# Optimization experiments

Hardware: AMD Instinct MI355X
Metric: run time of the kernel (lower is better)

The kernel has to match this reference:

```python
import jax, jax.numpy as jnp
import numpy as np
from jax import lax

B, CIN, CH, HW, K = 256, 256, 256, 16, 3


def setup_inputs() -> dict:
    key = jax.random.key(0)
    ks = jax.random.split(key, 9)
    s = 0.05
    return {
        "x": jax.random.normal(ks[0], (B, CIN, HW, HW), dtype=jnp.float32),
        "h": jax.random.normal(ks[1], (B, CH, HW, HW), dtype=jnp.float32),
        "c": jax.random.normal(ks[2], (B, CH, HW, HW), dtype=jnp.float32),
        # stacked x-branch conv weights for gates [i, f, c, o]; no bias (matches torch code)
        "Wx": jax.random.normal(ks[3], (4 * CH, CIN, K, K), dtype=jnp.float32) * s,
        # stacked h-branch conv weights for gates [i, f, c, o]; with bias
        "Wh": jax.random.normal(ks[4], (4 * CH, CH, K, K), dtype=jnp.float32) * s,
        "bh": jax.random.normal(ks[5], (4 * CH,), dtype=jnp.float32) * s,
        # peephole params (torch inits them to zeros; use small randn to exercise the math)
        "Wci": jax.random.normal(ks[6], (1, CH, HW, HW), dtype=jnp.float32) * s,
        "Wcf": jax.random.normal(ks[7], (1, CH, HW, HW), dtype=jnp.float32) * s,
        "Wco": jax.random.normal(ks[8], (1, CH, HW, HW), dtype=jnp.float32) * s,
    }


def _conv(x, w):
    # same-padding 2D conv, NCHW/OIHW
    return lax.conv_general_dilated(
        x, w, window_strides=(1, 1), padding="SAME",
        dimension_numbers=("NCHW", "OIHW", "NCHW"))


def reference(x, h, c, Wx, Wh, bh, Wci, Wcf, Wco):
    gx = _conv(x, Wx)                                   # [B, 4*CH, H, W]
    gh = _conv(h, Wh) + bh[None, :, None, None]         # [B, 4*CH, H, W]
    xi, xf, xc, xo = jnp.split(gx, 4, axis=1)
    hi, hf, hc, ho = jnp.split(gh, 4, axis=1)
    i_t = jax.nn.sigmoid(xi + hi + Wci * c)
    f_t = jax.nn.sigmoid(xf + hf + Wcf * c)
    c_t = f_t * c + i_t * jnp.tanh(xc + hc)
    o_t = jax.nn.sigmoid(xo + ho + Wco * c_t)
    h_t = o_t * jnp.tanh(c_t)
    return (h_t, c_t)
```

## Files before the change

kernel.cpp:

```cpp
#include <hip/hip_runtime.h>


typedef __bf16 bf16x8 __attribute__((ext_vector_type(8)));
typedef float f32x16 __attribute__((ext_vector_type(16)));

#define PLANE_B  20736u
#define XH_BYTES (4096u * PLANE_B)
#define OUT_HALF 16777216u

__device__ inline void gload_lds16(const void* g, void* l) {
    __builtin_amdgcn_global_load_lds(
        (const __attribute__((address_space(1))) void*)g,
        (__attribute__((address_space(3))) void*)l, 16, 0, 0);
}

__global__ __launch_bounds__(256) void xh_transform(
    const float* __restrict__ x, const float* __restrict__ hh,
    unsigned char* __restrict__ xh)
{
    int blk = blockIdx.x;
    int b = blk >> 4, ibk = blk & 15;
    const float* src = (ibk < 8) ? (x  + ((size_t)(b*256 + ibk*32)) * 256)
                                 : (hh + ((size_t)(b*256 + (ibk-8)*32)) * 256);
    int t = threadIdx.x;
    uint32_t w[16];
#pragma unroll
    for (int i = 0; i < 16; ++i) {
        __bf16 lo = (__bf16)src[(size_t)(2*i  )*256 + t];
        __bf16 hi = (__bf16)src[(size_t)(2*i+1)*256 + t];
        w[i] = (uint32_t)__builtin_bit_cast(unsigned short, lo)
             | ((uint32_t)__builtin_bit_cast(unsigned short, hi) << 16);
    }
    unsigned char* plane = xh + (size_t)blk * PLANE_B;
    int p = ((t >> 4) + 1)*18 + (t & 15) + 1;
    uint32_t key  = (uint32_t)(p & 7) << 4;
    uint32_t base = (uint32_t)p * 64u;
#pragma unroll
    for (int k = 0; k < 4; ++k)
        *(uint4*)(plane + ((base + 16u*k) ^ key)) =
            uint4{w[4*k], w[4*k+1], w[4*k+2], w[4*k+3]};
    if (t < 68) {
        int pb;
        if      (t < 18) pb = t;
        else if (t < 36) pb = 17*18 + (t - 18);
        else if (t < 52) pb = (t - 35)*18;
        else             pb = (t - 51)*18 + 17;
        uint32_t kb = (uint32_t)(pb & 7) << 4;
        uint32_t bb = (uint32_t)pb * 64u;
        uint4 z{0u,0u,0u,0u};
#pragma unroll
        for (int k = 0; k < 4; ++k)
            *(uint4*)(plane + ((bb + 16u*k) ^ kb)) = z;
    }
}

__global__ __launch_bounds__(256) void w_transform(
    const float* __restrict__ Wx, const float* __restrict__ Wh,
    __bf16* __restrict__ Wt)
{
    int idx  = blockIdx.x * 256 + threadIdx.x;
    int lane = idx & 63;
    int chunk = idx >> 6;
    int f    = chunk & 3;
    int half = (chunk >> 2) & 1;
    int pos  = (chunk >> 3) % 9;
    int rest = (chunk >> 3) / 9;
    int ibk  = rest & 15;
    int cb   = rest >> 4;
    int row = lane & 31, hl = lane >> 5;
    int gate = row & 3, ch8 = row >> 2;
    int oc  = gate*256 + cb*32 + f*8 + ch8;
    int ic0 = ibk*32 + half*16 + hl*8;
    bf16x8 v;
#pragma unroll
    for (int j = 0; j < 8; ++j) {
        int ic = ic0 + j;
        float w = (ic < 256) ? Wx[((size_t)oc*256 + ic      )*9 + pos]
                             : Wh[((size_t)oc*256 + (ic-256))*9 + pos];
        v[j] = (__bf16)w;
    }
    *(bf16x8*)(Wt + (size_t)chunk*512 + (size_t)lane*8) = v;
}

__global__ __launch_bounds__(256, 2) void convlstm_main(
    const unsigned char* __restrict__ xh, const unsigned char* __restrict__ Wtb,
    const float* __restrict__ bh,  const float* __restrict__ cin,
    const float* __restrict__ Wci, const float* __restrict__ Wcf,
    const float* __restrict__ Wco, float* __restrict__ out)
{
    int bid = blockIdx.x;
    int cb  = bid & 7;
    int b   = bid >> 3;
    int tid = threadIdx.x;
    int lane = tid & 63, wv = tid >> 6;
    int wm = wv & 1, wf = wv >> 1;
    int l31 = lane & 31, hl = lane >> 5;

    __shared__ __align__(16) unsigned char lds[2][24576];

    f32x16 acc[4][2];
#pragma unroll
    for (int j = 0; j < 2; ++j) {
        int fg = wf*2 + j;
        f32x16 v;
#pragma unroll
        for (int r = 0; r < 16; ++r) {
            int gate = r & 3, q = r >> 2;
            v[r] = bh[gate*256 + cb*32 + fg*8 + 2*q + hl];
        }
        acc[0][j] = v; acc[1][j] = v; acc[2][j] = v; acc[3][j] = v;
    }

    const unsigned char* planes = xh + (size_t)b * (16u * PLANE_B);

#pragma unroll
    for (int k = 0; k < 6; ++k)
        gload_lds16(planes + (size_t)(wv*6 + k)*1024u + (size_t)lane*16u,
                    &lds[0][(wv*6 + k)*1024 + lane*16]);

    int m0 = wm*128 + l31;
    int pb0 = (m0 >> 4)*18 + (m0 & 15);
    const uint32_t kbase = (uint32_t)(hl*16);
    uint32_t baddr[9][2];
#pragma unroll
    for (int pos = 0; pos < 9; ++pos) {
        int d = (pos/3)*18 + (pos%3);
        int pp = pb0 + d;
        uint32_t a = ((uint32_t)pp*64u + kbase) ^ (((uint32_t)(pp & 7)) << 4);
        baddr[pos][0] = a;
        baddr[pos][1] = (a + 2304u) ^ 64u;
    }
    const char* lds0 = (const char*)&lds[0][0];

    const unsigned char* aptr = Wtb + (size_t)cb*1179648u
                                    + (size_t)(wf*2048) + (size_t)(lane*16);

    bf16x8 A[3][2], Bb[2][4];
    A[0][0] = *(const bf16x8*)(aptr + 0);
    A[0][1] = *(const bf16x8*)(aptr + 1024);
    A[1][0] = *(const bf16x8*)(aptr + 4096);
    A[1][1] = *(const bf16x8*)(aptr + 5120);

    __syncthreads();

#define IBK_PHASES(LAST)                                                     \
    {                                                                        \
           \
        Bb[0][0] = *(const bf16x8*)(lds0 + baddr[0][0]);                     \
        Bb[0][1] = *(const bf16x8*)(lds0 + baddr[0][1]);                     \
        Bb[0][2] = *(const bf16x8*)(lds0 + baddr[0][0] + 4608);              \
        Bb[0][3] = *(const bf16x8*)(lds0 + baddr[0][1] + 4608);              \
        _Pragma("unroll")                                                    \
        for (int p = 0; p < 18; ++p) {                                       \
                                    \
            {                                                                \
                const int tp = p + 2;                                        \
                const int off = (tp < 18)                                    \
                    ? (tp*4096)                                              \
                    : ((LAST) ? (17*4096)                         \
                              : (73728 + (tp-18)*4096));                     \
                A[(p+2)%3][0] = *(const bf16x8*)(aptr + off);                \
                A[(p+2)%3][1] = *(const bf16x8*)(aptr + off + 1024);         \
            }                                                                \
            if (p == 1 && !(LAST)) {                                         \
                const unsigned char* np_ = planes + (size_t)(ibk+1)*PLANE_B; \
                _Pragma("unroll")                                            \
                for (int k = 0; k < 6; ++k)                                  \
                    gload_lds16(np_ + (size_t)(wv*6 + k)*1024u               \
                                    + (size_t)lane*16u,                      \
                                &lds[(ibk & 1) ^ 1][(wv*6 + k)*1024          \
                                                    + lane*16]);             \
            }                                                                \
                                \
            if (p < 17) {                                                    \
                const int np = p + 1;                                        \
                const uint32_t hx = (uint32_t)((np & 1)*32);                 \
                uint32_t a0 = baddr[np>>1][0] ^ hx;                          \
                uint32_t a1 = baddr[np>>1][1] ^ hx;                          \
                Bb[np&1][0] = *(const bf16x8*)(lds0 + a0);                   \
                Bb[np&1][1] = *(const bf16x8*)(lds0 + a1);                   \
                Bb[np&1][2] = *(const bf16x8*)(lds0 + a0 + 4608);            \
                Bb[np&1][3] = *(const bf16x8*)(lds0 + a1 + 4608);            \
            }                                                                \
            __builtin_amdgcn_s_setprio(1);                                   \
            acc[0][0] = __builtin_amdgcn_mfma_f32_32x32x16_bf16(A[p%3][0], Bb[p&1][0], acc[0][0], 0, 0, 0); \
            acc[0][1] = __builtin_amdgcn_mfma_f32_32x32x16_bf16(A[p%3][1], Bb[p&1][0], acc[0][1], 0, 0, 0); \
            acc[1][0] = __builtin_amdgcn_mfma_f32_32x32x16_bf16(A[p%3][0], Bb[p&1][1], acc[1][0], 0, 0, 0); \
            acc[1][1] = __builtin_amdgcn_mfma_f32_32x32x16_bf16(A[p%3][1], Bb[p&1][1], acc[1][1], 0, 0, 0); \
            acc[2][0] = __builtin_amdgcn_mfma_f32_32x32x16_bf16(A[p%3][0], Bb[p&1][2], acc[2][0], 0, 0, 0); \
            acc[2][1] = __builtin_amdgcn_mfma_f32_32x32x16_bf16(A[p%3][1], Bb[p&1][2], acc[2][1], 0, 0, 0); \
            acc[3][0] = __builtin_amdgcn_mfma_f32_32x32x16_bf16(A[p%3][0], Bb[p&1][3], acc[3][0], 0, 0, 0); \
            acc[3][1] = __builtin_amdgcn_mfma_f32_32x32x16_bf16(A[p%3][1], Bb[p&1][3], acc[3][1], 0, 0, 0); \
            __builtin_amdgcn_s_setprio(0);                                   \
        }                                                                    \
    }

    int flipd = 24576;
    for (int ibk = 0; ibk < 15; ++ibk) {
        IBK_PHASES(0)
#pragma unroll
        for (int pos = 0; pos < 9; ++pos) {
            baddr[pos][0] += (uint32_t)flipd;
            baddr[pos][1] += (uint32_t)flipd;
        }
        flipd = -flipd;
        aptr += 73728;
        asm volatile("s_waitcnt vmcnt(4) lgkmcnt(0)" ::: "memory");
        __builtin_amdgcn_s_barrier();
        __builtin_amdgcn_sched_barrier(0);
    }
    {
        const int ibk = 15;
        (void)ibk;
        IBK_PHASES(1)
    }
#undef IBK_PHASES

    float* outh = out;
    float* outc = out + (size_t)OUT_HALF;
    const size_t bOff = (size_t)b * (256*256);
#pragma unroll
    for (int mf = 0; mf < 4; ++mf) {
        int m = wm*128 + mf*32 + l31;
#pragma unroll
        for (int j = 0; j < 2; ++j) {
            int fg = wf*2 + j;
#pragma unroll
            for (int q = 0; q < 4; ++q) {
                int ch = cb*32 + fg*8 + 2*q + hl;
                size_t pidx = (size_t)ch*256 + (size_t)m;
                size_t idx  = bOff + pidx;
                float cv = cin[idx];
                float pi = acc[mf][j][4*q+0];
                float pf = acc[mf][j][4*q+1];
                float pc = acc[mf][j][4*q+2];
                float po = acc[mf][j][4*q+3];
                float it = 1.f/(1.f + __expf(-(pi + Wci[pidx]*cv)));
                float ft = 1.f/(1.f + __expf(-(pf + Wcf[pidx]*cv)));
                float tc = 1.f - 2.f/(1.f + __expf(2.f*pc));
                float ct = ft*cv + it*tc;
                float ot = 1.f/(1.f + __expf(-(po + Wco[pidx]*ct)));
                float th = 1.f - 2.f/(1.f + __expf(2.f*ct));
                outh[idx] = ot*th;
                outc[idx] = ct;
            }
        }
    }
}

extern "C" void kernel_launch(void* const* d_in, const int* in_sizes, int n_in,
                              void* d_out, int out_size, void* d_ws, size_t ws_size,
                              hipStream_t stream)
{
    const float* x   = (const float*)d_in[0];
    const float* h   = (const float*)d_in[1];
    const float* c   = (const float*)d_in[2];
    const float* Wx  = (const float*)d_in[3];
    const float* Wh  = (const float*)d_in[4];
    const float* bh  = (const float*)d_in[5];
    const float* Wci = (const float*)d_in[6];
    const float* Wcf = (const float*)d_in[7];
    const float* Wco = (const float*)d_in[8];
    float* out = (float*)d_out;

    unsigned char* xh = (unsigned char*)d_ws;
    unsigned char* wtb = xh + (size_t)XH_BYTES + 4096;

    hipLaunchKernelGGL(xh_transform, dim3(4096), dim3(256), 0, stream, x, h, xh);
    hipLaunchKernelGGL(w_transform,  dim3(2304), dim3(256), 0, stream,
                       Wx, Wh, (__bf16*)wtb);
    hipLaunchKernelGGL(convlstm_main, dim3(2048), dim3(256), 0, stream,
                       xh, wtb, bh, c, Wci, Wcf, Wco, out);
}
```

Measured before the change: 580.9 us.

## Triple-buffer LDS input planes and prefetch two iterations ahead

Grows the LDS staging from two plane buffers to three. Each input-channel block is now fetched two iterations ahead, and the first B fragments of the next block are read from LDS before the barrier. The end-of-iteration wait is relaxed to vmcnt(32) with no lgkmcnt drain, so the global-to-LDS copy latency has more time to hide behind MFMA work. The cost is 72KB of LDS per block, which leaves little headroom for two blocks per CU, plus more complex rotating buffer-offset bookkeeping.

```diff
diff --git a/kernel.cpp b/kernel.cpp
--- a/kernel.cpp
+++ b/kernel.cpp
@@ -7,6 +7,7 @@
 #define PLANE_B  20736u
 #define XH_BYTES (4096u * PLANE_B)
 #define OUT_HALF 16777216u
+#define BUFSTEP  24576
 
 __device__ inline void gload_lds16(const void* g, void* l) {
     __builtin_amdgcn_global_load_lds(
@@ -96,7 +97,7 @@
     int wm = wv & 1, wf = wv >> 1;
     int l31 = lane & 31, hl = lane >> 5;
 
-    __shared__ __align__(16) unsigned char lds[2][24576];
+    __shared__ __align__(16) unsigned char lds3[3*24576];
 
     f32x16 acc[4][2];
 #pragma unroll
@@ -114,9 +115,13 @@
     const unsigned char* planes = xh + (size_t)b * (16u * PLANE_B);
 
 #pragma unroll
-    for (int k = 0; k < 6; ++k)
+    for (int k = 0; k < 6; ++k) {
         gload_lds16(planes + (size_t)(wv*6 + k)*1024u + (size_t)lane*16u,
-                    &lds[0][(wv*6 + k)*1024 + lane*16]);
+                    &lds3[(wv*6 + k)*1024 + lane*16]);
+        gload_lds16(planes + PLANE_B + (size_t)(wv*6 + k)*1024u
+                           + (size_t)lane*16u,
+                    &lds3[BUFSTEP + (wv*6 + k)*1024 + lane*16]);
+    }
 
     int m0 = wm*128 + l31;
     int pb0 = (m0 >> 4)*18 + (m0 & 15);
@@ -130,7 +135,7 @@
         baddr[pos][0] = a;
         baddr[pos][1] = (a + 2304u) ^ 64u;
     }
-    const char* lds0 = (const char*)&lds[0][0];
+    const char* lds0 = (const char*)&lds3[0];
 
     const unsigned char* aptr = Wtb + (size_t)cb*1179648u
                                     + (size_t)(wf*2048) + (size_t)(lane*16);
@@ -143,13 +148,17 @@
 
     __syncthreads();
 
+    Bb[0][0] = *(const bf16x8*)(lds0 + baddr[0][0]);
+    Bb[0][1] = *(const bf16x8*)(lds0 + baddr[0][1]);
+    Bb[0][2] = *(const bf16x8*)(lds0 + baddr[0][0] + 4608);
+    Bb[0][3] = *(const bf16x8*)(lds0 + baddr[0][1] + 4608);
+
+    int delta  = BUFSTEP;
+    int bof    = 0;
+    int dmaoff = 2*BUFSTEP;
+
 #define IBK_PHASES(LAST)                                                     \
     {                                                                        \
-           \
-        Bb[0][0] = *(const bf16x8*)(lds0 + baddr[0][0]);                     \
-        Bb[0][1] = *(const bf16x8*)(lds0 + baddr[0][1]);                     \
-        Bb[0][2] = *(const bf16x8*)(lds0 + baddr[0][0] + 4608);              \
-        Bb[0][3] = *(const bf16x8*)(lds0 + baddr[0][1] + 4608);              \
         _Pragma("unroll")                                                    \
         for (int p = 0; p < 18; ++p) {                                       \
                                     \
@@ -162,16 +171,16 @@
                 A[(p+2)%3][0] = *(const bf16x8*)(aptr + off);                \
                 A[(p+2)%3][1] = *(const bf16x8*)(aptr + off + 1024);         \
             }                                                                \
-            if (p == 1 && !(LAST)) {                                         \
-                const unsigned char* np_ = planes + (size_t)(ibk+1)*PLANE_B; \
+                              \
+            if (p == 1 && !(LAST) && ibk <= 13) {                            \
+                const unsigned char* np_ = planes + (size_t)(ibk+2)*PLANE_B; \
                 _Pragma("unroll")                                            \
                 for (int k = 0; k < 6; ++k)                                  \
                     gload_lds16(np_ + (size_t)(wv*6 + k)*1024u               \
                                     + (size_t)lane*16u,                      \
-                                &lds[(ibk & 1) ^ 1][(wv*6 + k)*1024          \
-                                                    + lane*16]);             \
+                                &lds3[dmaoff + (wv*6 + k)*1024 + lane*16]);  \
             }                                                                \
-                                \
+                                       \
             if (p < 17) {                                                    \
                 const int np = p + 1;                                        \
                 const uint32_t hx = (uint32_t)((np & 1)*32);                 \
@@ -181,6 +190,13 @@
                 Bb[np&1][1] = *(const bf16x8*)(lds0 + a1);                   \
                 Bb[np&1][2] = *(const bf16x8*)(lds0 + a0 + 4608);            \
                 Bb[np&1][3] = *(const bf16x8*)(lds0 + a1 + 4608);            \
+            } else if (!(LAST)) {                                            \
+                uint32_t a0n = baddr[0][0] + (uint32_t)delta;                \
+                uint32_t a1n = baddr[0][1] + (uint32_t)delta;                \
+                Bb[0][0] = *(const bf16x8*)(lds0 + a0n);                     \
+                Bb[0][1] = *(const bf16x8*)(lds0 + a1n);                     \
+                Bb[0][2] = *(const bf16x8*)(lds0 + a0n + 4608);              \
+                Bb[0][3] = *(const bf16x8*)(lds0 + a1n + 4608);              \
             }                                                                \
             __builtin_amdgcn_s_setprio(1);                                   \
             acc[0][0] = __builtin_amdgcn_mfma_f32_32x32x16_bf16(A[p%3][0], Bb[p&1][0], acc[0][0], 0, 0, 0); \
@@ -195,17 +211,18 @@
         }                                                                    \
     }
 
-    int flipd = 24576;
     for (int ibk = 0; ibk < 15; ++ibk) {
         IBK_PHASES(0)
 #pragma unroll
         for (int pos = 0; pos < 9; ++pos) {
-            baddr[pos][0] += (uint32_t)flipd;
-            baddr[pos][1] += (uint32_t)flipd;
+            baddr[pos][0] += (uint32_t)delta;
+            baddr[pos][1] += (uint32_t)delta;
         }
-        flipd = -flipd;
         aptr += 73728;
-        asm volatile("s_waitcnt vmcnt(4) lgkmcnt(0)" ::: "memory");
+        bof += delta;
+        delta  = (bof == 2*BUFSTEP) ? -(2*BUFSTEP) : BUFSTEP;
+        dmaoff = (dmaoff == 2*BUFSTEP) ? 0 : dmaoff + BUFSTEP;
+        asm volatile("s_waitcnt vmcnt(32)" ::: "memory");
         __builtin_amdgcn_s_barrier();
         __builtin_amdgcn_sched_barrier(0);
     }
```

Result: no change. 579.5 us (-0.2%).
